# Kernel optimization log

Hardware: AMD Instinct MI355X
Metric: run time of the kernel (lower is better)

The kernel has to match this reference:

```python
import jax, jax.numpy as jnp
import numpy as np

TEMP = 0.1
EPS = 1e-12


def setup_inputs() -> dict:
    key = jax.random.key(0)
    k0, k1 = jax.random.split(key)
    instances_view0 = jax.random.normal(k0, (128, 32, 512), dtype=jnp.float32)
    instances_view1 = jax.random.normal(k1, (128, 32, 512), dtype=jnp.float32)
    return {"instances_view0": instances_view0, "instances_view1": instances_view1}


def reference(instances_view0, instances_view1):
    B, I, D = instances_view0.shape
    n_per_view = B * I  # n_instances_per_view
    f0 = instances_view0.reshape(n_per_view, D)
    f1 = instances_view1.reshape(n_per_view, D)
    inst = jnp.concatenate((f0, f1), axis=0)  # [N, D], N = 2*B*I
    # L2 normalize rows (torch F.normalize with eps clamp)
    norm = jnp.maximum(jnp.linalg.norm(inst, axis=1, keepdims=True), EPS)
    z = inst / norm
    sim_exp = jnp.exp(z @ z.T / TEMP)  # [N, N]
    denom = sim_exp.sum(axis=1) - jnp.diagonal(sim_exp)  # exclude self-similarity
    # positives: pairs offset by n_per_view in both directions
    idx = jnp.arange(n_per_view)
    upper = sim_exp[idx, idx + n_per_view]   # diagonal(offset=+n)
    lower = sim_exp[idx + n_per_view, idx]   # diagonal(offset=-n)
    nom = jnp.concatenate((upper, lower), axis=0)  # [N]
    loss = -jnp.log(nom / denom)
    return loss.mean()  # reduction='batchmean'
```

## Files before the change

kernel.cpp:

```cpp
#include <hip/hip_runtime.h>
#include <hip/hip_bf16.h>
#include <cstdint>

#define NROWS 8192
#define NPER  4096
#define DIM   512
#define TEMP_INV 10.0f
#define FP8_SCALE 16.0f
#define DOT_UNSCALE (1.0f / 256.0f)
#define NB    64
#define NBLK  2080
#define PAIR_OFF 32

typedef float f32x4 __attribute__((ext_vector_type(4)));
typedef long  lx2   __attribute__((ext_vector_type(2)));

__global__ __launch_bounds__(256) void k_normalize(const float* __restrict__ v0,
                                                   const float* __restrict__ v1,
                                                   unsigned char* __restrict__ z,
                                                   float* __restrict__ rowsum,
                                                   float* __restrict__ out) {
  if (blockIdx.x < 32) rowsum[blockIdx.x * 256 + threadIdx.x] = 0.f;
  if (blockIdx.x == 0 && threadIdx.x == 0) out[0] = 0.f;
  const int wid  = (blockIdx.x * 256 + threadIdx.x) >> 6;
  const int lane = threadIdx.x & 63;
  if (wid >= NROWS) return;
  const float* src = (wid < NPER) ? (v0 + (size_t)wid * DIM)
                                  : (v1 + (size_t)(wid - NPER) * DIM);
  float4 a = *(const float4*)(src + lane * 8);
  float4 b = *(const float4*)(src + lane * 8 + 4);
  float ss = a.x*a.x + a.y*a.y + a.z*a.z + a.w*a.w
           + b.x*b.x + b.y*b.y + b.z*b.z + b.w*b.w;
  #pragma unroll
  for (int m = 1; m < 64; m <<= 1) ss += __shfl_xor(ss, m);
  float inv = FP8_SCALE / fmaxf(sqrtf(ss), 1e-12f);
  int w0 = __builtin_amdgcn_cvt_pk_fp8_f32(a.x * inv, a.y * inv, 0, false);
  w0     = __builtin_amdgcn_cvt_pk_fp8_f32(a.z * inv, a.w * inv, w0, true);
  int w1 = __builtin_amdgcn_cvt_pk_fp8_f32(b.x * inv, b.y * inv, 0, false);
  w1     = __builtin_amdgcn_cvt_pk_fp8_f32(b.z * inv, b.w * inv, w1, true);
  uint2 p; p.x = (unsigned)w0; p.y = (unsigned)w1;
  *(uint2*)(z + (size_t)wid * DIM + lane * 8) = p;
}

__global__ __launch_bounds__(256, 3) void k_gemm_sym(const unsigned char* __restrict__ z,
                                                     float* __restrict__ rowsum,
                                                     float* __restrict__ s) {
  __shared__ __align__(16) unsigned char As[128 * 128];
  __shared__ __align__(16) unsigned char Bs[128 * 128];

  const int tid  = threadIdx.x;
  const int lane = tid & 63;
  const int w    = tid >> 6;
  const int wr   = w >> 1;
  const int wc   = w & 1;

  const int orig = blockIdx.x;
  const int t = (orig & 7) * (NBLK / 8) + (orig >> 3);

  int a = 0;
  while (a < 7 && 484 * (a + 1) - 32 * (a + 1) * a <= t) ++a;
  int l = t - (484 * a - 32 * a * (a - 1));
  int ri, rj, sj;
  if (l < 36) {
    sj = a;
    ri = 0;
    while (l >= 8 - ri) { l -= 8 - ri; ++ri; }
    rj = ri + l;
  } else {
    l -= 36;
    sj = a + 1 + (l >> 6);
    const int ll = l & 63;
    ri = ll >> 3; rj = ll & 7;
  }
  const int bi = a * 8 + ri;
  const int bj = sj * 8 + rj;
  const int brow = bi * 128;
  const int bcol = bj * 128;
  const bool diag = (bi == bj);
  const bool pair = (bj - bi == PAIR_OFF);

  f32x4 acc[4][4];
  const f32x4 zero = {0.f, 0.f, 0.f, 0.f};
  #pragma unroll
  for (int m = 0; m < 4; ++m)
    #pragma unroll
    for (int n = 0; n < 4; ++n) acc[m][n] = zero;

  const int srow = (lane >> 3);
  const int skof = 16 * ((lane & 7) ^ srow);
  auto stage = [&](int k0) {
    #pragma unroll
    for (int i = 0; i < 4; ++i) {
      const int c = w * 4 + i;
      const int row_in = c * 8 + srow;
      const unsigned char* ga = z + (size_t)(brow + row_in) * DIM + k0 + skof;
      const unsigned char* gb = z + (size_t)(bcol + row_in) * DIM + k0 + skof;
      __builtin_amdgcn_global_load_lds(
          (const __attribute__((address_space(1))) void*)ga,
          (__attribute__((address_space(3))) void*)(&As[c * 1024]), 16, 0, 0);
      __builtin_amdgcn_global_load_lds(
          (const __attribute__((address_space(1))) void*)gb,
          (__attribute__((address_space(3))) void*)(&Bs[c * 1024]), 16, 0, 0);
    }
  };

  const int r0 = lane & 15;
  const int g  = lane >> 4;

  for (int kt = 0; kt < 4; ++kt) {
    stage(kt * 128);
    asm volatile("s_waitcnt vmcnt(0)" ::: "memory");
    __builtin_amdgcn_s_barrier();

    const char* Ab = (const char*)&As[0] + (size_t)(wr * 64 + r0) * 128;
    const char* Bb = (const char*)&Bs[0] + (size_t)(wc * 64 + r0) * 128;
    #pragma unroll
    for (int p = 0; p < 2; ++p) {
      const int cb = (((2 * g + p) ^ (r0 & 7)) << 4);
      lx2 bfrag[4];
      #pragma unroll
      for (int n = 0; n < 4; ++n)
        bfrag[n] = *(const lx2*)(Bb + n * (16 * 128) + cb);
      #pragma unroll
      for (int m = 0; m < 4; ++m) {
        lx2 afrag = *(const lx2*)(Ab + m * (16 * 128) + cb);
        #pragma unroll
        for (int n = 0; n < 4; ++n) {
          acc[m][n] = __builtin_amdgcn_mfma_f32_16x16x32_fp8_fp8(
              afrag[0], bfrag[n][0], acc[m][n], 0, 0, 0);
          acc[m][n] = __builtin_amdgcn_mfma_f32_16x16x32_fp8_fp8(
              afrag[1], bfrag[n][1], acc[m][n], 0, 0, 0);
        }
      }
    }
    asm volatile("s_waitcnt lgkmcnt(0)" ::: "memory");
    __builtin_amdgcn_sched_barrier(0);
    __builtin_amdgcn_s_barrier();
  }

  float (*racc)[128] = (float (*)[128])As;
  float (*cacc)[128] = ((float (*)[128])As) + 2;

  float cs[4] = {0.f, 0.f, 0.f, 0.f};
  const int grow0 = brow + wr * 64;
  const int gcol0 = bcol + wc * 64;
  const float expc = TEMP_INV * DOT_UNSCALE;
  #pragma unroll
  for (int m = 0; m < 4; ++m) {
    #pragma unroll
    for (int j = 0; j < 4; ++j) {
      const int grow = grow0 + m * 16 + g * 4 + j;
      float v = 0.f;
      #pragma unroll
      for (int n = 0; n < 4; ++n) {
        const int gcol = gcol0 + n * 16 + r0;
        const float rawacc = acc[m][n][j];
        const float e = __expf(rawacc * expc);
        if (grow != gcol) { v += e; cs[n] += e; }
        if (pair && (grow + NPER == gcol)) {
          const float raw = rawacc * DOT_UNSCALE;
          s[grow] = raw;
          s[gcol] = raw;
        }
      }
      v += __shfl_xor(v, 1);
      v += __shfl_xor(v, 2);
      v += __shfl_xor(v, 4);
      v += __shfl_xor(v, 8);
      if (r0 == 0) racc[wc][wr * 64 + m * 16 + g * 4 + j] = v;
    }
  }
  #pragma unroll
  for (int n = 0; n < 4; ++n) {
    float v = cs[n];
    v += __shfl_xor(v, 16);
    v += __shfl_xor(v, 32);
    if (lane < 16) cacc[wr][wc * 64 + n * 16 + lane] = v;
  }
  __syncthreads();
  if (tid < 128) {
    atomicAdd(&rowsum[brow + tid], racc[0][tid] + racc[1][tid]);
  } else if (!diag) {
    const int i = tid - 128;
    atomicAdd(&rowsum[bcol + i], cacc[0][i] + cacc[1][i]);
  }
}

__global__ __launch_bounds__(256) void k_loss(const float* __restrict__ rowsum,
                                              const float* __restrict__ s,
                                              float* __restrict__ out) {
  __shared__ float red[4];
  const int i = blockIdx.x * 256 + threadIdx.x;
  float v = logf(rowsum[i]) - s[i] * TEMP_INV;
  #pragma unroll
  for (int m = 1; m < 64; m <<= 1) v += __shfl_xor(v, m);
  const int w = threadIdx.x >> 6;
  if ((threadIdx.x & 63) == 0) red[w] = v;
  __syncthreads();
  if (threadIdx.x == 0)
    atomicAdd(out, (red[0] + red[1] + red[2] + red[3]) * (1.0f / (float)NROWS));
}

extern "C" void kernel_launch(void* const* d_in, const int* in_sizes, int n_in,
                              void* d_out, int out_size, void* d_ws, size_t ws_size,
                              hipStream_t stream) {
  const float* v0 = (const float*)d_in[0];
  const float* v1 = (const float*)d_in[1];
  float* out = (float*)d_out;

  unsigned char* z = (unsigned char*)d_ws;
  float* rowsum = (float*)((char*)d_ws + (size_t)NROWS * DIM);
  float* s      = rowsum + NROWS;

  k_normalize<<<NROWS / 4, 256, 0, stream>>>(v0, v1, z, rowsum, out);
  k_gemm_sym<<<NBLK, 256, 0, stream>>>(z, rowsum, s);
  k_loss<<<NROWS / 256, 256, 0, stream>>>(rowsum, s, out);
}
```

Baseline: 48.96 us.

## Double-buffer A tile in LDS and load B fragments directly from global

The A operand tile is now double-buffered in shared memory, with two K-slices prefetched up front and later slices issued after each compute step, so global loads overlap the MFMA work. The B operand no longer goes through LDS: each wave loads its B fragments straight from global memory into registers every K-step. The aim is to hide load latency and cut LDS traffic, at the cost of more global and L2 traffic for B (duplicated across waves) and more register pressure. The k-permutation is changed consistently for A and B so the dot products still match.

```diff
diff --git a/kernel.cpp b/kernel.cpp
--- a/kernel.cpp
+++ b/kernel.cpp
@@ -45,8 +45,7 @@
 __global__ __launch_bounds__(256, 3) void k_gemm_sym(const unsigned char* __restrict__ z,
                                                      float* __restrict__ rowsum,
                                                      float* __restrict__ s) {
-  __shared__ __align__(16) unsigned char As[128 * 128];
-  __shared__ __align__(16) unsigned char Bs[128 * 128];
+  __shared__ __align__(16) unsigned char As[2][128 * 128];
 
   const int tid  = threadIdx.x;
   const int lane = tid & 63;
@@ -88,54 +87,62 @@
 
   const int srow = (lane >> 3);
   const int skof = 16 * ((lane & 7) ^ srow);
-  auto stage = [&](int k0) {
+  auto stageA = [&](int buf, int k0) {
     #pragma unroll
     for (int i = 0; i < 4; ++i) {
       const int c = w * 4 + i;
       const int row_in = c * 8 + srow;
       const unsigned char* ga = z + (size_t)(brow + row_in) * DIM + k0 + skof;
-      const unsigned char* gb = z + (size_t)(bcol + row_in) * DIM + k0 + skof;
       __builtin_amdgcn_global_load_lds(
           (const __attribute__((address_space(1))) void*)ga,
-          (__attribute__((address_space(3))) void*)(&As[c * 1024]), 16, 0, 0);
-      __builtin_amdgcn_global_load_lds(
-          (const __attribute__((address_space(1))) void*)gb,
-          (__attribute__((address_space(3))) void*)(&Bs[c * 1024]), 16, 0, 0);
+          (__attribute__((address_space(3))) void*)(&As[buf][c * 1024]), 16, 0, 0);
     }
   };
 
   const int r0 = lane & 15;
   const int g  = lane >> 4;
-
+  const unsigned char* zB = z + (size_t)(bcol + wc * 64 + r0) * DIM + g * 16;
+
+  stageA(0, 0);
+  stageA(1, 128);
+
+  #pragma unroll
   for (int kt = 0; kt < 4; ++kt) {
-    stage(kt * 128);
-    asm volatile("s_waitcnt vmcnt(0)" ::: "memory");
+    const int cur = kt & 1;
+    const int k0 = kt * 128;
+    if (kt < 3) asm volatile("s_waitcnt vmcnt(4)" ::: "memory");
+    else        asm volatile("s_waitcnt vmcnt(0)" ::: "memory");
     __builtin_amdgcn_s_barrier();
 
-    const char* Ab = (const char*)&As[0] + (size_t)(wr * 64 + r0) * 128;
-    const char* Bb = (const char*)&Bs[0] + (size_t)(wc * 64 + r0) * 128;
+    lx2 bq[4][2];
+    #pragma unroll
+    for (int n = 0; n < 4; ++n)
+      #pragma unroll
+      for (int p = 0; p < 2; ++p)
+        bq[n][p] = *(const lx2*)(zB + (size_t)(n * 16) * DIM + k0 + p * 64);
+    __builtin_amdgcn_sched_barrier(0);
+
+    const char* Ab = (const char*)&As[cur][0] + (size_t)(wr * 64 + r0) * 128;
     #pragma unroll
     for (int p = 0; p < 2; ++p) {
-      const int cb = (((2 * g + p) ^ (r0 & 7)) << 4);
-      lx2 bfrag[4];
-      #pragma unroll
-      for (int n = 0; n < 4; ++n)
-        bfrag[n] = *(const lx2*)(Bb + n * (16 * 128) + cb);
-      #pragma unroll
-      for (int m = 0; m < 4; ++m) {
-        lx2 afrag = *(const lx2*)(Ab + m * (16 * 128) + cb);
+      lx2 aq[4];
+      #pragma unroll
+      for (int m = 0; m < 4; ++m)
+        aq[m] = *(const lx2*)(Ab + m * (16 * 128) + (((g + 4 * p) ^ (r0 & 7)) << 4));
+      #pragma unroll
+      for (int m = 0; m < 4; ++m)
         #pragma unroll
         for (int n = 0; n < 4; ++n) {
           acc[m][n] = __builtin_amdgcn_mfma_f32_16x16x32_fp8_fp8(
-              afrag[0], bfrag[n][0], acc[m][n], 0, 0, 0);
+              aq[m][0], bq[n][p][0], acc[m][n], 0, 0, 0);
           acc[m][n] = __builtin_amdgcn_mfma_f32_16x16x32_fp8_fp8(
-              afrag[1], bfrag[n][1], acc[m][n], 0, 0, 0);
+              aq[m][1], bq[n][p][1], acc[m][n], 0, 0, 0);
         }
-      }
     }
     asm volatile("s_waitcnt lgkmcnt(0)" ::: "memory");
     __builtin_amdgcn_sched_barrier(0);
     __builtin_amdgcn_s_barrier();
+    if (kt < 2) stageA(cur, (kt + 2) * 128);
   }
 
   float (*racc)[128] = (float (*)[128])As;
```

Measured after the change: 62.04 us. 26.7% more time.
